# Kernel optimization log

Hardware: AMD Instinct MI355X
Metric: run time of the kernel (lower is better)

## Reference

```python
import jax, jax.numpy as jnp
import numpy as np

B, L1, L, DIM_IN, DIM_H, DIM_M = 8, 64, 1024, 512, 512, 512


def setup_inputs() -> dict:
    key = jax.random.key(0)
    ks = jax.random.split(key, 7)
    return {
        "query": jax.random.normal(ks[0], (L1, DIM_H), dtype=jnp.float32),
        "keys": jax.random.normal(ks[1], (B, L, DIM_IN), dtype=jnp.float32),
        "values": jax.random.normal(ks[2], (B, L, DIM_IN), dtype=jnp.float32),
        # nn.Linear weights: Wx (dim_middle, dim_in) no bias; Wh (dim_middle, dim_h) with bias; w (dim_middle,) no bias
        "Wx": jax.random.normal(ks[3], (DIM_M, DIM_IN), dtype=jnp.float32) * 0.02,
        "Wh": jax.random.normal(ks[4], (DIM_M, DIM_H), dtype=jnp.float32) * 0.02,
        "bh": jax.random.normal(ks[5], (DIM_M,), dtype=jnp.float32) * 0.02,
        "w": jax.random.normal(ks[6], (DIM_M,), dtype=jnp.float32) * 0.02,
    }


def reference(query, keys, values, Wx, Wh, bh, w):
    # mode='concept': query [l1, dh], keys/values [b, l, d]
    kx = jnp.einsum('bld,md->blm', keys, Wx)          # [b, l, m]
    qh = jnp.einsum('qd,md->qm', query, Wh) + bh       # [l1, m]
    g = jax.nn.relu(kx[:, None, :, :] + qh[None, :, None, :])  # [b, l1, l, m]
    scores = jnp.einsum('bqlm,m->bql', g, w)           # [b, l1, l]
    e = jax.nn.softmax(scores, axis=-1)                # softmax over key len (dim 2)
    return jnp.einsum('bql,bld->bqd', e, values)       # [b, l1, dv]
```

## Files before the change

kernel.cpp:

```cpp
#include <hip/hip_runtime.h>
#include <hip/hip_bf16.h>

#define BB 8
#define L1 64
#define LL 1024
#define DD 512

typedef float f32x4 __attribute__((ext_vector_type(4)));
typedef _Float16 f16;
typedef _Float16 f16x2 __attribute__((ext_vector_type(2)));
typedef _Float16 f16x4 __attribute__((ext_vector_type(4)));
typedef _Float16 f16x8 __attribute__((ext_vector_type(8)));

union F16x8u { f16x8 v; f16x2 h[4]; };

__global__ __launch_bounds__(256, 2) void kxqh_kernel(
    const float* __restrict__ keys,
    const float* __restrict__ query,
    const float* __restrict__ Wx,
    const float* __restrict__ Wh,
    const float* __restrict__ bh,
    f16* __restrict__ kx,
    f16* __restrict__ qh) {
  __shared__ char lds[24576] __attribute__((aligned(128)));
  const int t = threadIdx.x;
  const int lane = t & 63;
  const int w = t >> 6;
  const int wr = w >> 1, wc = w & 1;
  const int fq = lane >> 4, fr = lane & 15;
  const int bid = blockIdx.x;
  const bool isQH = (bid >= 512);
  const int rt = isQH ? 0 : (bid & 63);
  const int mt = isQH ? (bid - 512) : (bid >> 6);
  const int rowA0 = rt * 128;
  const int m0 = mt * 64;
  const float* Ap = isQH ? query : keys;
  const float* Wp = isQH ? Wh : Wx;

  f32x4 acc[4][2] = {};
  float4 ra[8], rb[4];

#define LOADK(K0)                                                              \
  do {                                                                         \
    _Pragma("unroll") for (int i = 0; i < 8; ++i) {                            \
      int flat = t * 4 + i * 1024;                                             \
      int row = flat >> 6, col = flat & 63;                                    \
      int arow = isQH ? (row & 63) : (rowA0 + row);                            \
      ra[i] = *reinterpret_cast<const float4*>(Ap + (size_t)arow * DD + (K0) + col); \
    }                                                                          \
    _Pragma("unroll") for (int i = 0; i < 4; ++i) {                            \
      int flat = t * 4 + i * 1024;                                             \
      int row = flat >> 6, col = flat & 63;                                    \
      rb[i] = *reinterpret_cast<const float4*>(Wp + (size_t)(m0 + row) * DD + (K0) + col); \
    }                                                                          \
  } while (0)

  LOADK(0);
  for (int s = 0; s < 8; ++s) {
    #pragma unroll
    for (int i = 0; i < 8; ++i) {
      int flat = t * 4 + i * 1024;
      int row = flat >> 6, col = flat & 63;
      f16x4 ha;
      ha[0] = (f16)ra[i].x; ha[1] = (f16)ra[i].y; ha[2] = (f16)ra[i].z; ha[3] = (f16)ra[i].w;
      int byte = (row * 128 + col * 2) ^ ((row & 7) << 4);
      *reinterpret_cast<f16x4*>(lds + byte) = ha;
    }
    #pragma unroll
    for (int i = 0; i < 4; ++i) {
      int flat = t * 4 + i * 1024;
      int row = flat >> 6, col = flat & 63;
      f16x4 hb;
      hb[0] = (f16)rb[i].x; hb[1] = (f16)rb[i].y; hb[2] = (f16)rb[i].z; hb[3] = (f16)rb[i].w;
      int byte = 16384 + ((row * 128 + col * 2) ^ ((row & 7) << 4));
      *reinterpret_cast<f16x4*>(lds + byte) = hb;
    }
    if (s < 7) LOADK((s + 1) * 64);
    __syncthreads();
    #pragma unroll
    for (int kh = 0; kh < 2; ++kh) {
      f16x8 af[4], bf[2];
      #pragma unroll
      for (int mi = 0; mi < 4; ++mi) {
        int row = wr * 64 + mi * 16 + fr;
        int byte = (row * 128 + kh * 64 + fq * 16) ^ ((row & 7) << 4);
        af[mi] = *reinterpret_cast<const f16x8*>(lds + byte);
      }
      #pragma unroll
      for (int ni = 0; ni < 2; ++ni) {
        int row = wc * 32 + ni * 16 + fr;
        int byte = 16384 + ((row * 128 + kh * 64 + fq * 16) ^ ((row & 7) << 4));
        bf[ni] = *reinterpret_cast<const f16x8*>(lds + byte);
      }
      #pragma unroll
      for (int mi = 0; mi < 4; ++mi)
        #pragma unroll
        for (int ni = 0; ni < 2; ++ni)
          acc[mi][ni] = __builtin_amdgcn_mfma_f32_16x16x32_f16(
              af[mi], bf[ni], acc[mi][ni], 0, 0, 0);
    }
    __syncthreads();
  }
#undef LOADK
  if (isQH) {
    #pragma unroll
    for (int mi = 0; mi < 4; ++mi) {
      #pragma unroll
      for (int ni = 0; ni < 2; ++ni) {
        int row = wr * 64 + mi * 16 + fq * 4;
        int col = m0 + wc * 32 + ni * 16 + fr;
        if (row < 64) {
          float bias = bh[col];
          #pragma unroll
          for (int r = 0; r < 4; ++r)
            qh[(size_t)(row + r) * DD + col] = (f16)(acc[mi][ni][r] + bias);
        }
      }
    }
  } else {
    #pragma unroll
    for (int mi = 0; mi < 4; ++mi) {
      #pragma unroll
      for (int ni = 0; ni < 2; ++ni) {
        int row = rowA0 + wr * 64 + mi * 16 + fq * 4;
        int col = m0 + wc * 32 + ni * 16 + fr;
        #pragma unroll
        for (int r = 0; r < 4; ++r)
          kx[(size_t)(row + r) * DD + col] = (f16)acc[mi][ni][r];
      }
    }
  }
}

__global__ __launch_bounds__(256, 2) void score4_kernel(
    const f16* __restrict__ kx,
    const f16* __restrict__ qh,
    const float* __restrict__ w,
    float* __restrict__ sc,
    float* __restrict__ pmax) {
  const int b = blockIdx.x & 7;
  const int l0 = (blockIdx.x >> 3) * 32;
  const int t = threadIdx.x;
  __shared__ __align__(16) f16 kxs[32][136];
  __shared__ __align__(16) f16 qhs[64][136];
  __shared__ __align__(16) f16 wsf[DD];
  __shared__ float smax[64][17];
  if (t < 128) {
    float4 wv = *reinterpret_cast<const float4*>(w + t * 4);
    f16x4 hv; hv[0] = (f16)wv.x; hv[1] = (f16)wv.y; hv[2] = (f16)wv.z; hv[3] = (f16)wv.w;
    *reinterpret_cast<f16x4*>(&wsf[t * 4]) = hv;
  }
  const int qb = t & 15;
  const int lt = (t >> 4) * 2;
  float acc[2][4] = {};
  uint4 rkx[2], rqh[4];

#define LOADM(M0)                                                              \
  do {                                                                         \
    _Pragma("unroll") for (int p = 0; p < 2; ++p) {                            \
      int flat = t * 8 + p * 2048;                                             \
      int row = flat >> 7, col = flat & 127;                                   \
      rkx[p] = *reinterpret_cast<const uint4*>(kx + (size_t)(b * LL + l0 + row) * DD + (M0) + col); \
    }                                                                          \
    _Pragma("unroll") for (int p = 0; p < 4; ++p) {                            \
      int flat = t * 8 + p * 2048;                                             \
      int row = flat >> 7, col = flat & 127;                                   \
      rqh[p] = *reinterpret_cast<const uint4*>(qh + (size_t)row * DD + (M0) + col); \
    }                                                                          \
  } while (0)

  LOADM(0);
  for (int m0 = 0; m0 < DD; m0 += 128) {
    #pragma unroll
    for (int p = 0; p < 2; ++p) {
      int flat = t * 8 + p * 2048;
      int row = flat >> 7, col = flat & 127;
      *reinterpret_cast<uint4*>(&kxs[row][col]) = rkx[p];
    }
    #pragma unroll
    for (int p = 0; p < 4; ++p) {
      int flat = t * 8 + p * 2048;
      int row = flat >> 7, col = flat & 127;
      *reinterpret_cast<uint4*>(&qhs[row][col]) = rqh[p];
    }
    if (m0 < DD - 128) LOADM(m0 + 128);
    __syncthreads();
    #pragma unroll 2
    for (int mm = 0; mm < 128; mm += 8) {
      F16x8u kv0, kv1, wv;
      kv0.v = *reinterpret_cast<const f16x8*>(&kxs[lt][mm]);
      kv1.v = *reinterpret_cast<const f16x8*>(&kxs[lt + 1][mm]);
      wv.v = *reinterpret_cast<const f16x8*>(&wsf[m0 + mm]);
      #pragma unroll
      for (int j = 0; j < 4; ++j) {
        F16x8u qv, g0, g1;
        qv.v = *reinterpret_cast<const f16x8*>(&qhs[qb + 16 * j][mm]);
        f16x8 zz = {};
        g0.v = __builtin_elementwise_max(kv0.v + qv.v, zz);
        g1.v = __builtin_elementwise_max(kv1.v + qv.v, zz);
        #pragma unroll
        for (int c = 0; c < 4; ++c) {
          acc[0][j] = __builtin_amdgcn_fdot2(g0.h[c], wv.h[c], acc[0][j], false);
          acc[1][j] = __builtin_amdgcn_fdot2(g1.h[c], wv.h[c], acc[1][j], false);
        }
      }
    }
    __syncthreads();
  }
#undef LOADM
  #pragma unroll
  for (int i = 0; i < 2; ++i)
    #pragma unroll
    for (int j = 0; j < 4; ++j)
      sc[((size_t)b * L1 + qb + 16 * j) * LL + l0 + lt + i] = acc[i][j];
  #pragma unroll
  for (int j = 0; j < 4; ++j)
    smax[qb + 16 * j][t >> 4] = fmaxf(acc[0][j], acc[1][j]);
  __syncthreads();
  if (t < 64) {
    float m = smax[t][0];
    #pragma unroll
    for (int i = 1; i < 16; ++i) m = fmaxf(m, smax[t][i]);
    pmax[((size_t)b * L1 + t) * 32 + (l0 >> 5)] = m;
  }
}

__global__ __launch_bounds__(256) void fso_kernel(
    const float* __restrict__ sc,
    const float* __restrict__ pmax,
    const float* __restrict__ v,
    float* __restrict__ out) {
  __shared__ __align__(16) char es[64 * 256];
  __shared__ __align__(16) char vt[16 * 256];
  __shared__ float rowm[64];
  __shared__ float rowinv[64];
  __shared__ float spart[64][17];
  const int t = threadIdx.x;
  const int lane = t & 63;
  const int w = t >> 6;
  const int fq = lane >> 4, fr = lane & 15;
  const int bid = blockIdx.x;
  const int b = bid & 7;
  const int d0 = (bid >> 3) * 16;
  const float* scb = sc + (size_t)b * L1 * LL;
  const float* vb = v + (size_t)b * LL * DD;

  const int eq = t >> 4;
  const int ec8 = t & 15;
  const int vl = t >> 1;
  const int vdh = (t & 1) * 8;
  float4 rsc[4][2];
  float4 rv[2];

#define LOADC(LC)                                                              \
  do {                                                                         \
    _Pragma("unroll") for (int p = 0; p < 4; ++p) {                            \
      const float* src = scb + (size_t)(eq + p * 16) * LL + (LC) * 128 + ec8 * 8; \
      rsc[p][0] = *reinterpret_cast<const float4*>(src);                       \
      rsc[p][1] = *reinterpret_cast<const float4*>(src + 4);                   \
    }                                                                          \
    const float* vsrc = vb + (size_t)((LC) * 128 + vl) * DD + d0 + vdh;        \
    rv[0] = *reinterpret_cast<const float4*>(vsrc);                            \
    rv[1] = *reinterpret_cast<const float4*>(vsrc + 4);                        \
  } while (0)

  LOADC(0);
  if (t < 64) {
    const float* pm = pmax + ((size_t)b * L1 + t) * 32;
    float4 m4 = *reinterpret_cast<const float4*>(pm);
    #pragma unroll
    for (int i = 1; i < 8; ++i) {
      float4 x = *reinterpret_cast<const float4*>(pm + i * 4);
      m4.x = fmaxf(m4.x, x.x); m4.y = fmaxf(m4.y, x.y);
      m4.z = fmaxf(m4.z, x.z); m4.w = fmaxf(m4.w, x.w);
    }
    rowm[t] = fmaxf(fmaxf(m4.x, m4.y), fmaxf(m4.z, m4.w));
  }
  __syncthreads();
  float rmv[4];
  #pragma unroll
  for (int p = 0; p < 4; ++p) rmv[p] = rowm[eq + p * 16];
  float spp[4] = {0.f, 0.f, 0.f, 0.f};
  f32x4 acc = {};

  for (int c = 0; c < 8; ++c) {
    #pragma unroll
    for (int p = 0; p < 4; ++p) {
      int q = eq + p * 16;
      float xs[8] = {rsc[p][0].x, rsc[p][0].y, rsc[p][0].z, rsc[p][0].w,
                     rsc[p][1].x, rsc[p][1].y, rsc[p][1].z, rsc[p][1].w};
      f16x8 h;
      #pragma unroll
      for (int j = 0; j < 8; ++j) {
        float e = __expf(xs[j] - rmv[p]);
        spp[p] += e;
        h[j] = (f16)e;
      }
      int byte = q * 256 + ((ec8 * 16) ^ ((q & 7) << 4));
      *reinterpret_cast<f16x8*>(es + byte) = h;
    }
    {
      float vs[8] = {rv[0].x, rv[0].y, rv[0].z, rv[0].w,
                     rv[1].x, rv[1].y, rv[1].z, rv[1].w};
      #pragma unroll
      for (int j = 0; j < 8; ++j) {
        int d = vdh + j;
        int byte = d * 256 + ((2 * vl) ^ ((d & 7) << 4));
        *reinterpret_cast<f16*>(vt + byte) = (f16)vs[j];
      }
    }
    if (c < 7) LOADC(c + 1);
    __syncthreads();
    #pragma unroll
    for (int ks = 0; ks < 4; ++ks) {
      int qa = w * 16 + fr;
      int colb = ks * 64 + fq * 16;
      f16x8 a = *reinterpret_cast<const f16x8*>(es + qa * 256 + (colb ^ ((qa & 7) << 4)));
      f16x8 bb = *reinterpret_cast<const f16x8*>(vt + fr * 256 + (colb ^ ((fr & 7) << 4)));
      acc = __builtin_amdgcn_mfma_f32_16x16x32_f16(a, bb, acc, 0, 0, 0);
    }
    __syncthreads();
  }
#undef LOADC
  #pragma unroll
  for (int p = 0; p < 4; ++p) spart[eq + p * 16][ec8] = spp[p];
  __syncthreads();
  if (t < 64) {
    float S = 0.f;
    #pragma unroll
    for (int i = 0; i < 16; ++i) S += spart[t][i];
    rowinv[t] = 1.f / S;
  }
  __syncthreads();
  #pragma unroll
  for (int r = 0; r < 4; ++r) {
    int q = w * 16 + fq * 4 + r;
    out[((size_t)b * L1 + q) * DD + d0 + fr] = acc[r] * rowinv[q];
  }
}

extern "C" void kernel_launch(void* const* d_in, const int* in_sizes, int n_in,
                              void* d_out, int out_size, void* d_ws, size_t ws_size,
                              hipStream_t stream) {
  const float* query  = (const float*)d_in[0];
  const float* keys   = (const float*)d_in[1];
  const float* values = (const float*)d_in[2];
  const float* Wx     = (const float*)d_in[3];
  const float* Wh     = (const float*)d_in[4];
  const float* bh     = (const float*)d_in[5];
  const float* w      = (const float*)d_in[6];
  float* out = (float*)d_out;

  char* ws = (char*)d_ws;
  f16*   kx   = (f16*)ws;
  f16*   qh   = (f16*)(ws + 8388608);
  float* sc   = (float*)(ws + 8454144);
  float* pmax = (float*)(ws + 10551296);

  kxqh_kernel<<<520, 256, 0, stream>>>(keys, query, Wx, Wh, bh, kx, qh);
  score4_kernel<<<BB * (LL / 32), 256, 0, stream>>>(kx, qh, w, sc, pmax);
  fso_kernel<<<256, 256, 0, stream>>>(sc, pmax, values, out);
}
```

Before: 59.50 us.

## Fuse keys projection into score kernel, split small qh GEMM into own kernel

```diff
diff --git a/kernel.cpp b/kernel.cpp
--- a/kernel.cpp
+++ b/kernel.cpp
@@ -14,187 +14,193 @@
 
 union F16x8u { f16x8 v; f16x2 h[4]; };
 
-__global__ __launch_bounds__(256, 2) void kxqh_kernel(
-    const float* __restrict__ keys,
+__global__ __launch_bounds__(256) void qh_kernel(
     const float* __restrict__ query,
-    const float* __restrict__ Wx,
     const float* __restrict__ Wh,
     const float* __restrict__ bh,
-    f16* __restrict__ kx,
     f16* __restrict__ qh) {
-  __shared__ char lds[24576] __attribute__((aligned(128)));
+  __shared__ char lds[18432] __attribute__((aligned(128)));
   const int t = threadIdx.x;
   const int lane = t & 63;
-  const int w = t >> 6;
-  const int wr = w >> 1, wc = w & 1;
+  const int wid = t >> 6;
   const int fq = lane >> 4, fr = lane & 15;
-  const int bid = blockIdx.x;
-  const bool isQH = (bid >= 512);
-  const int rt = isQH ? 0 : (bid & 63);
-  const int mt = isQH ? (bid - 512) : (bid >> 6);
-  const int rowA0 = rt * 128;
-  const int m0 = mt * 64;
-  const float* Ap = isQH ? query : keys;
-  const float* Wp = isQH ? Wh : Wx;
-
-  f32x4 acc[4][2] = {};
-  float4 ra[8], rb[4];
-
-#define LOADK(K0)                                                              \
+  const int m0 = blockIdx.x * 64;
+  f32x4 acc[4] = {};
+  float4 rq[4], rw[4];
+
+#define LOADQ(KC)                                                              \
   do {                                                                         \
-    _Pragma("unroll") for (int i = 0; i < 8; ++i) {                            \
-      int flat = t * 4 + i * 1024;                                             \
-      int row = flat >> 6, col = flat & 63;                                    \
-      int arow = isQH ? (row & 63) : (rowA0 + row);                            \
-      ra[i] = *reinterpret_cast<const float4*>(Ap + (size_t)arow * DD + (K0) + col); \
-    }                                                                          \
     _Pragma("unroll") for (int i = 0; i < 4; ++i) {                            \
-      int flat = t * 4 + i * 1024;                                             \
-      int row = flat >> 6, col = flat & 63;                                    \
-      rb[i] = *reinterpret_cast<const float4*>(Wp + (size_t)(m0 + row) * DD + (K0) + col); \
+      int slot = t + i * 256;                                                  \
+      int row = slot >> 4, c4 = (slot & 15) * 4;                               \
+      rq[i] = *reinterpret_cast<const float4*>(query + (size_t)row * DD + (KC)*64 + c4); \
+      rw[i] = *reinterpret_cast<const float4*>(Wh + (size_t)(m0 + row) * DD + (KC)*64 + c4); \
     }                                                                          \
   } while (0)
 
-  LOADK(0);
-  for (int s = 0; s < 8; ++s) {
-    #pragma unroll
-    for (int i = 0; i < 8; ++i) {
-      int flat = t * 4 + i * 1024;
-      int row = flat >> 6, col = flat & 63;
-      f16x4 ha;
-      ha[0] = (f16)ra[i].x; ha[1] = (f16)ra[i].y; ha[2] = (f16)ra[i].z; ha[3] = (f16)ra[i].w;
-      int byte = (row * 128 + col * 2) ^ ((row & 7) << 4);
-      *reinterpret_cast<f16x4*>(lds + byte) = ha;
-    }
+  LOADQ(0);
+  for (int kc = 0; kc < 8; ++kc) {
     #pragma unroll
     for (int i = 0; i < 4; ++i) {
-      int flat = t * 4 + i * 1024;
-      int row = flat >> 6, col = flat & 63;
-      f16x4 hb;
-      hb[0] = (f16)rb[i].x; hb[1] = (f16)rb[i].y; hb[2] = (f16)rb[i].z; hb[3] = (f16)rb[i].w;
-      int byte = 16384 + ((row * 128 + col * 2) ^ ((row & 7) << 4));
-      *reinterpret_cast<f16x4*>(lds + byte) = hb;
-    }
-    if (s < 7) LOADK((s + 1) * 64);
+      int slot = t + i * 256;
+      int row = slot >> 4, c4 = (slot & 15) * 4;
+      f16x4 hq, hw;
+      hq[0] = (f16)rq[i].x; hq[1] = (f16)rq[i].y; hq[2] = (f16)rq[i].z; hq[3] = (f16)rq[i].w;
+      hw[0] = (f16)rw[i].x; hw[1] = (f16)rw[i].y; hw[2] = (f16)rw[i].z; hw[3] = (f16)rw[i].w;
+      *reinterpret_cast<f16x4*>(lds + row * 144 + c4 * 2) = hq;
+      *reinterpret_cast<f16x4*>(lds + 9216 + row * 144 + c4 * 2) = hw;
+    }
+    if (kc < 7) LOADQ(kc + 1);
     __syncthreads();
     #pragma unroll
     for (int kh = 0; kh < 2; ++kh) {
-      f16x8 af[4], bf[2];
-      #pragma unroll
-      for (int mi = 0; mi < 4; ++mi) {
-        int row = wr * 64 + mi * 16 + fr;
-        int byte = (row * 128 + kh * 64 + fq * 16) ^ ((row & 7) << 4);
-        af[mi] = *reinterpret_cast<const f16x8*>(lds + byte);
-      }
-      #pragma unroll
-      for (int ni = 0; ni < 2; ++ni) {
-        int row = wc * 32 + ni * 16 + fr;
-        int byte = 16384 + ((row * 128 + kh * 64 + fq * 16) ^ ((row & 7) << 4));
-        bf[ni] = *reinterpret_cast<const f16x8*>(lds + byte);
-      }
-      #pragma unroll
-      for (int mi = 0; mi < 4; ++mi)
-        #pragma unroll
-        for (int ni = 0; ni < 2; ++ni)
-          acc[mi][ni] = __builtin_amdgcn_mfma_f32_16x16x32_f16(
-              af[mi], bf[ni], acc[mi][ni], 0, 0, 0);
-    }
-    __syncthreads();
-  }
-#undef LOADK
-  if (isQH) {
-    #pragma unroll
-    for (int mi = 0; mi < 4; ++mi) {
-      #pragma unroll
-      for (int ni = 0; ni < 2; ++ni) {
-        int row = wr * 64 + mi * 16 + fq * 4;
-        int col = m0 + wc * 32 + ni * 16 + fr;
-        if (row < 64) {
-          float bias = bh[col];
-          #pragma unroll
-          for (int r = 0; r < 4; ++r)
-            qh[(size_t)(row + r) * DD + col] = (f16)(acc[mi][ni][r] + bias);
-        }
-      }
-    }
-  } else {
-    #pragma unroll
-    for (int mi = 0; mi < 4; ++mi) {
-      #pragma unroll
-      for (int ni = 0; ni < 2; ++ni) {
-        int row = rowA0 + wr * 64 + mi * 16 + fq * 4;
-        int col = m0 + wc * 32 + ni * 16 + fr;
-        #pragma unroll
-        for (int r = 0; r < 4; ++r)
-          kx[(size_t)(row + r) * DD + col] = (f16)acc[mi][ni][r];
-      }
-    }
+      f16x8 bf = *reinterpret_cast<const f16x8*>(
+          lds + 9216 + (wid * 16 + fr) * 144 + kh * 64 + fq * 16);
+      #pragma unroll
+      for (int qf = 0; qf < 4; ++qf) {
+        f16x8 af = *reinterpret_cast<const f16x8*>(
+            lds + (qf * 16 + fr) * 144 + kh * 64 + fq * 16);
+        acc[qf] = __builtin_amdgcn_mfma_f32_16x16x32_f16(af, bf, acc[qf], 0, 0, 0);
+      }
+    }
+    __syncthreads();
+  }
+#undef LOADQ
+  #pragma unroll
+  for (int qf = 0; qf < 4; ++qf) {
+    int m = m0 + wid * 16 + fr;
+    float bias = bh[m];
+    #pragma unroll
+    for (int r = 0; r < 4; ++r)
+      qh[(size_t)(qf * 16 + fq * 4 + r) * DD + m] = (f16)(acc[qf][r] + bias);
   }
 }
 
-__global__ __launch_bounds__(256, 2) void score4_kernel(
-    const f16* __restrict__ kx,
+#define KEYSH_OFF 0
+#define WXS_OFF   32768
+#define QHS_OFF   32768
+#define KXS_OFF   51200
+#define WSF_OFF   59904
+#define SMAX_OFF  60928
+
+__global__ __launch_bounds__(256) void kscore_kernel(
+    const float* __restrict__ keys,
     const f16* __restrict__ qh,
+    const float* __restrict__ Wx,
     const float* __restrict__ w,
     float* __restrict__ sc,
     float* __restrict__ pmax) {
+  __shared__ char lds[63232] __attribute__((aligned(128)));
+  const int t = threadIdx.x;
+  const int lane = t & 63;
+  const int wid = t >> 6;
+  const int fq = lane >> 4, fr = lane & 15;
   const int b = blockIdx.x & 7;
   const int l0 = (blockIdx.x >> 3) * 32;
-  const int t = threadIdx.x;
-  __shared__ __align__(16) f16 kxs[32][136];
-  __shared__ __align__(16) f16 qhs[64][136];
-  __shared__ __align__(16) f16 wsf[DD];
-  __shared__ float smax[64][17];
+  const int qb = t & 15;
+  const int lq = t >> 4;
+
+  #pragma unroll
+  for (int j = 0; j < 16; ++j) {
+    int slot = t + j * 256;
+    int l = slot >> 7, kcol = (slot & 127) * 4;
+    float4 kv = *reinterpret_cast<const float4*>(
+        keys + (size_t)(b * LL + l0 + l) * DD + kcol);
+    f16x4 h;
+    h[0] = (f16)kv.x; h[1] = (f16)kv.y; h[2] = (f16)kv.z; h[3] = (f16)kv.w;
+    *reinterpret_cast<f16x4*>(
+        lds + KEYSH_OFF + l * 1024 + ((kcol * 2) ^ ((l & 7) << 4))) = h;
+  }
   if (t < 128) {
     float4 wv = *reinterpret_cast<const float4*>(w + t * 4);
     f16x4 hv; hv[0] = (f16)wv.x; hv[1] = (f16)wv.y; hv[2] = (f16)wv.z; hv[3] = (f16)wv.w;
-    *reinterpret_cast<f16x4*>(&wsf[t * 4]) = hv;
-  }
-  const int qb = t & 15;
-  const int lt = (t >> 4) * 2;
-  float acc[2][4] = {};
-  uint4 rkx[2], rqh[4];
-
-#define LOADM(M0)                                                              \
+    *reinterpret_cast<f16x4*>(lds + WSF_OFF + t * 8) = hv;
+  }
+
+  float4 rb[8];
+#define LOADW(MC, KC)                                                          \
   do {                                                                         \
-    _Pragma("unroll") for (int p = 0; p < 2; ++p) {                            \
-      int flat = t * 8 + p * 2048;                                             \
-      int row = flat >> 7, col = flat & 127;                                   \
-      rkx[p] = *reinterpret_cast<const uint4*>(kx + (size_t)(b * LL + l0 + row) * DD + (M0) + col); \
-    }                                                                          \
-    _Pragma("unroll") for (int p = 0; p < 4; ++p) {                            \
-      int flat = t * 8 + p * 2048;                                             \
-      int row = flat >> 7, col = flat & 127;                                   \
-      rqh[p] = *reinterpret_cast<const uint4*>(qh + (size_t)row * DD + (M0) + col); \
+    _Pragma("unroll") for (int i = 0; i < 8; ++i) {                            \
+      int slot = t + i * 256;                                                  \
+      int m = slot >> 4, c4 = (slot & 15) * 4;                                 \
+      rb[i] = *reinterpret_cast<const float4*>(                                \
+          Wx + (size_t)((MC) * 128 + m) * DD + (KC) * 64 + c4);                \
     }                                                                          \
   } while (0)
 
-  LOADM(0);
-  for (int m0 = 0; m0 < DD; m0 += 128) {
-    #pragma unroll
-    for (int p = 0; p < 2; ++p) {
-      int flat = t * 8 + p * 2048;
-      int row = flat >> 7, col = flat & 127;
-      *reinterpret_cast<uint4*>(&kxs[row][col]) = rkx[p];
-    }
-    #pragma unroll
-    for (int p = 0; p < 4; ++p) {
-      int flat = t * 8 + p * 2048;
-      int row = flat >> 7, col = flat & 127;
-      *reinterpret_cast<uint4*>(&qhs[row][col]) = rqh[p];
-    }
-    if (m0 < DD - 128) LOADM(m0 + 128);
+  LOADW(0, 0);
+  float acc[2][4] = {};
+
+  for (int mc = 0; mc < 4; ++mc) {
+    f32x4 cacc[2][2] = {};
+    for (int kc = 0; kc < 8; ++kc) {
+      #pragma unroll
+      for (int i = 0; i < 8; ++i) {
+        int slot = t + i * 256;
+        int m = slot >> 4, c4 = (slot & 15) * 4;
+        f16x4 h;
+        h[0] = (f16)rb[i].x; h[1] = (f16)rb[i].y; h[2] = (f16)rb[i].z; h[3] = (f16)rb[i].w;
+        *reinterpret_cast<f16x4*>(lds + WXS_OFF + m * 144 + c4 * 2) = h;
+      }
+      {
+        int nmc = mc, nkc = kc + 1;
+        if (nkc == 8) { nmc++; nkc = 0; }
+        if (nmc < 4) LOADW(nmc, nkc);
+      }
+      __syncthreads();
+      #pragma unroll
+      for (int kh = 0; kh < 2; ++kh) {
+        f16x8 af[2], bf[2];
+        #pragma unroll
+        for (int lf = 0; lf < 2; ++lf) {
+          int l = lf * 16 + fr;
+          af[lf] = *reinterpret_cast<const f16x8*>(
+              lds + KEYSH_OFF + l * 1024 +
+              ((kc * 128 + kh * 64 + fq * 16) ^ ((l & 7) << 4)));
+        }
+        #pragma unroll
+        for (int mf = 0; mf < 2; ++mf)
+          bf[mf] = *reinterpret_cast<const f16x8*>(
+              lds + WXS_OFF + (wid * 32 + mf * 16 + fr) * 144 + kh * 64 + fq * 16);
+        #pragma unroll
+        for (int lf = 0; lf < 2; ++lf)
+          #pragma unroll
+          for (int mf = 0; mf < 2; ++mf)
+            cacc[lf][mf] = __builtin_amdgcn_mfma_f32_16x16x32_f16(
+                af[lf], bf[mf], cacc[lf][mf], 0, 0, 0);
+      }
+      __syncthreads();
+    }
+    #pragma unroll
+    for (int lf = 0; lf < 2; ++lf)
+      #pragma unroll
+      for (int mf = 0; mf < 2; ++mf)
+        #pragma unroll
+        for (int r = 0; r < 4; ++r) {
+          int l = lf * 16 + fq * 4 + r;
+          int m = wid * 32 + mf * 16 + fr;
+          *reinterpret_cast<f16*>(lds + KXS_OFF + l * 272 + m * 2) =
+              (f16)cacc[lf][mf][r];
+        }
+    #pragma unroll
+    for (int j = 0; j < 4; ++j) {
+      int slot = t + j * 256;
+      int row = slot >> 4, c8 = (slot & 15) * 8;
+      uint4 qv = *reinterpret_cast<const uint4*>(qh + (size_t)row * DD + mc * 128 + c8);
+      *reinterpret_cast<uint4*>(lds + QHS_OFF + row * 272 + c8 * 2) = qv;
+    }
     __syncthreads();
     #pragma unroll 2
     for (int mm = 0; mm < 128; mm += 8) {
       F16x8u kv0, kv1, wv;
-      kv0.v = *reinterpret_cast<const f16x8*>(&kxs[lt][mm]);
-      kv1.v = *reinterpret_cast<const f16x8*>(&kxs[lt + 1][mm]);
-      wv.v = *reinterpret_cast<const f16x8*>(&wsf[m0 + mm]);
+      kv0.v = *reinterpret_cast<const f16x8*>(lds + KXS_OFF + lq * 272 + mm * 2);
+      kv1.v = *reinterpret_cast<const f16x8*>(lds + KXS_OFF + (lq + 16) * 272 + mm * 2);
+      wv.v = *reinterpret_cast<const f16x8*>(lds + WSF_OFF + (mc * 128 + mm) * 2);
       #pragma unroll
       for (int j = 0; j < 4; ++j) {
         F16x8u qv, g0, g1;
-        qv.v = *reinterpret_cast<const f16x8*>(&qhs[qb + 16 * j][mm]);
+        qv.v = *reinterpret_cast<const f16x8*>(
+            lds + QHS_OFF + (qb + 16 * j) * 272 + mm * 2);
         f16x8 zz = {};
         g0.v = __builtin_elementwise_max(kv0.v + qv.v, zz);
         g1.v = __builtin_elementwise_max(kv1.v + qv.v, zz);
@@ -207,20 +213,23 @@
     }
     __syncthreads();
   }
-#undef LOADM
+#undef LOADW
   #pragma unroll
   for (int i = 0; i < 2; ++i)
     #pragma unroll
     for (int j = 0; j < 4; ++j)
-      sc[((size_t)b * L1 + qb + 16 * j) * LL + l0 + lt + i] = acc[i][j];
+      sc[((size_t)b * L1 + qb + 16 * j) * LL + l0 + lq + 16 * i] = acc[i][j];
   #pragma unroll
   for (int j = 0; j < 4; ++j)
-    smax[qb + 16 * j][t >> 4] = fmaxf(acc[0][j], acc[1][j]);
+    *reinterpret_cast<f16*>(lds + SMAX_OFF + ((qb + 16 * j) * 18 + lq) * 2) =
+        (f16)fmaxf(acc[0][j], acc[1][j]);
   __syncthreads();
   if (t < 64) {
-    float m = smax[t][0];
-    #pragma unroll
-    for (int i = 1; i < 16; ++i) m = fmaxf(m, smax[t][i]);
+    float m = -3.4e38f;
+    #pragma unroll
+    for (int i = 0; i < 16; ++i)
+      m = fmaxf(m, (float)*reinterpret_cast<const f16*>(
+                       lds + SMAX_OFF + (t * 18 + i) * 2));
     pmax[((size_t)b * L1 + t) * 32 + (l0 >> 5)] = m;
   }
 }
@@ -352,12 +361,11 @@
   float* out = (float*)d_out;
 
   char* ws = (char*)d_ws;
-  f16*   kx   = (f16*)ws;
-  f16*   qh   = (f16*)(ws + 8388608);
-  float* sc   = (float*)(ws + 8454144);
-  float* pmax = (float*)(ws + 10551296);
-
-  kxqh_kernel<<<520, 256, 0, stream>>>(keys, query, Wx, Wh, bh, kx, qh);
-  score4_kernel<<<BB * (LL / 32), 256, 0, stream>>>(kx, qh, w, sc, pmax);
+  f16*   qh   = (f16*)ws;
+  float* sc   = (float*)(ws + 65536);
+  float* pmax = (float*)(ws + 65536 + 2097152);
+
+  qh_kernel<<<8, 256, 0, stream>>>(query, Wh, bh, qh);
+  kscore_kernel<<<256, 256, 0, stream>>>(keys, qh, Wx, w, sc, pmax);
   fso_kernel<<<256, 256, 0, stream>>>(sc, pmax, values, out);
 }
```

New measurement: 58.69 us. Within noise of the previous version (-1.4%).

## Split qh projection into own kernel and enlarge kx GEMM tile with double-buffered LDS

Applied to the files above, without the earlier changes.

```diff
diff --git a/kernel.cpp b/kernel.cpp
--- a/kernel.cpp
+++ b/kernel.cpp
@@ -14,120 +14,145 @@
 
 union F16x8u { f16x8 v; f16x2 h[4]; };
 
-__global__ __launch_bounds__(256, 2) void kxqh_kernel(
-    const float* __restrict__ keys,
+__global__ __launch_bounds__(256) void qh_kernel(
     const float* __restrict__ query,
-    const float* __restrict__ Wx,
     const float* __restrict__ Wh,
     const float* __restrict__ bh,
-    f16* __restrict__ kx,
     f16* __restrict__ qh) {
-  __shared__ char lds[24576] __attribute__((aligned(128)));
+  __shared__ char lds[18432] __attribute__((aligned(128)));
+  const int t = threadIdx.x;
+  const int lane = t & 63;
+  const int wid = t >> 6;
+  const int fq = lane >> 4, fr = lane & 15;
+  const int m0 = blockIdx.x * 64;
+  f32x4 acc[4] = {};
+  float4 rq[4], rw[4];
+
+#define LOADQ(KC)                                                              \
+  do {                                                                         \
+    _Pragma("unroll") for (int i = 0; i < 4; ++i) {                            \
+      int slot = t + i * 256;                                                  \
+      int row = slot >> 4, c4 = (slot & 15) * 4;                               \
+      rq[i] = *reinterpret_cast<const float4*>(query + (size_t)row * DD + (KC)*64 + c4); \
+      rw[i] = *reinterpret_cast<const float4*>(Wh + (size_t)(m0 + row) * DD + (KC)*64 + c4); \
+    }                                                                          \
+  } while (0)
+
+  LOADQ(0);
+  for (int kc = 0; kc < 8; ++kc) {
+    #pragma unroll
+    for (int i = 0; i < 4; ++i) {
+      int slot = t + i * 256;
+      int row = slot >> 4, c4 = (slot & 15) * 4;
+      f16x4 hq, hw;
+      hq[0] = (f16)rq[i].x; hq[1] = (f16)rq[i].y; hq[2] = (f16)rq[i].z; hq[3] = (f16)rq[i].w;
+      hw[0] = (f16)rw[i].x; hw[1] = (f16)rw[i].y; hw[2] = (f16)rw[i].z; hw[3] = (f16)rw[i].w;
+      *reinterpret_cast<f16x4*>(lds + row * 144 + c4 * 2) = hq;
+      *reinterpret_cast<f16x4*>(lds + 9216 + row * 144 + c4 * 2) = hw;
+    }
+    if (kc < 7) LOADQ(kc + 1);
+    __syncthreads();
+    #pragma unroll
+    for (int kh = 0; kh < 2; ++kh) {
+      f16x8 bf = *reinterpret_cast<const f16x8*>(
+          lds + 9216 + (wid * 16 + fr) * 144 + kh * 64 + fq * 16);
+      #pragma unroll
+      for (int qf = 0; qf < 4; ++qf) {
+        f16x8 af = *reinterpret_cast<const f16x8*>(
+            lds + (qf * 16 + fr) * 144 + kh * 64 + fq * 16);
+        acc[qf] = __builtin_amdgcn_mfma_f32_16x16x32_f16(af, bf, acc[qf], 0, 0, 0);
+      }
+    }
+    __syncthreads();
+  }
+#undef LOADQ
+  #pragma unroll
+  for (int qf = 0; qf < 4; ++qf) {
+    int m = m0 + wid * 16 + fr;
+    float bias = bh[m];
+    #pragma unroll
+    for (int r = 0; r < 4; ++r)
+      qh[(size_t)(qf * 16 + fq * 4 + r) * DD + m] = (f16)(acc[qf][r] + bias);
+  }
+}
+
+__global__ __launch_bounds__(256) void kx_kernel(
+    const float* __restrict__ keys,
+    const float* __restrict__ Wx,
+    f16* __restrict__ kx) {
+  __shared__ char lds[65536] __attribute__((aligned(128)));
   const int t = threadIdx.x;
   const int lane = t & 63;
   const int w = t >> 6;
   const int wr = w >> 1, wc = w & 1;
   const int fq = lane >> 4, fr = lane & 15;
-  const int bid = blockIdx.x;
-  const bool isQH = (bid >= 512);
-  const int rt = isQH ? 0 : (bid & 63);
-  const int mt = isQH ? (bid - 512) : (bid >> 6);
+  const int rt = blockIdx.x & 63;
+  const int mt = blockIdx.x >> 6;
   const int rowA0 = rt * 128;
-  const int m0 = mt * 64;
-  const float* Ap = isQH ? query : keys;
-  const float* Wp = isQH ? Wh : Wx;
-
-  f32x4 acc[4][2] = {};
-  float4 ra[8], rb[4];
+  const int m0 = mt * 128;
+
+  f32x4 acc[4][4] = {};
+  float4 ra[8], rb[8];
 
 #define LOADK(K0)                                                              \
   do {                                                                         \
     _Pragma("unroll") for (int i = 0; i < 8; ++i) {                            \
       int flat = t * 4 + i * 1024;                                             \
       int row = flat >> 6, col = flat & 63;                                    \
-      int arow = isQH ? (row & 63) : (rowA0 + row);                            \
-      ra[i] = *reinterpret_cast<const float4*>(Ap + (size_t)arow * DD + (K0) + col); \
-    }                                                                          \
-    _Pragma("unroll") for (int i = 0; i < 4; ++i) {                            \
-      int flat = t * 4 + i * 1024;                                             \
-      int row = flat >> 6, col = flat & 63;                                    \
-      rb[i] = *reinterpret_cast<const float4*>(Wp + (size_t)(m0 + row) * DD + (K0) + col); \
+      ra[i] = *reinterpret_cast<const float4*>(keys + (size_t)(rowA0 + row) * DD + (K0) + col); \
+      rb[i] = *reinterpret_cast<const float4*>(Wx + (size_t)(m0 + row) * DD + (K0) + col); \
     }                                                                          \
   } while (0)
 
   LOADK(0);
   for (int s = 0; s < 8; ++s) {
+    const int base = (s & 1) * 32768;
     #pragma unroll
     for (int i = 0; i < 8; ++i) {
       int flat = t * 4 + i * 1024;
       int row = flat >> 6, col = flat & 63;
-      f16x4 ha;
+      f16x4 ha, hb;
       ha[0] = (f16)ra[i].x; ha[1] = (f16)ra[i].y; ha[2] = (f16)ra[i].z; ha[3] = (f16)ra[i].w;
+      hb[0] = (f16)rb[i].x; hb[1] = (f16)rb[i].y; hb[2] = (f16)rb[i].z; hb[3] = (f16)rb[i].w;
       int byte = (row * 128 + col * 2) ^ ((row & 7) << 4);
-      *reinterpret_cast<f16x4*>(lds + byte) = ha;
-    }
-    #pragma unroll
-    for (int i = 0; i < 4; ++i) {
-      int flat = t * 4 + i * 1024;
-      int row = flat >> 6, col = flat & 63;
-      f16x4 hb;
-      hb[0] = (f16)rb[i].x; hb[1] = (f16)rb[i].y; hb[2] = (f16)rb[i].z; hb[3] = (f16)rb[i].w;
-      int byte = 16384 + ((row * 128 + col * 2) ^ ((row & 7) << 4));
-      *reinterpret_cast<f16x4*>(lds + byte) = hb;
+      *reinterpret_cast<f16x4*>(lds + base + byte) = ha;
+      *reinterpret_cast<f16x4*>(lds + base + 16384 + byte) = hb;
     }
     if (s < 7) LOADK((s + 1) * 64);
     __syncthreads();
     #pragma unroll
     for (int kh = 0; kh < 2; ++kh) {
-      f16x8 af[4], bf[2];
+      f16x8 af[4], bf[4];
       #pragma unroll
       for (int mi = 0; mi < 4; ++mi) {
         int row = wr * 64 + mi * 16 + fr;
         int byte = (row * 128 + kh * 64 + fq * 16) ^ ((row & 7) << 4);
-        af[mi] = *reinterpret_cast<const f16x8*>(lds + byte);
-      }
-      #pragma unroll
-      for (int ni = 0; ni < 2; ++ni) {
-        int row = wc * 32 + ni * 16 + fr;
-        int byte = 16384 + ((row * 128 + kh * 64 + fq * 16) ^ ((row & 7) << 4));
-        bf[ni] = *reinterpret_cast<const f16x8*>(lds + byte);
+        af[mi] = *reinterpret_cast<const f16x8*>(lds + base + byte);
+      }
+      #pragma unroll
+      for (int ni = 0; ni < 4; ++ni) {
+        int row = wc * 64 + ni * 16 + fr;
+        int byte = (row * 128 + kh * 64 + fq * 16) ^ ((row & 7) << 4);
+        bf[ni] = *reinterpret_cast<const f16x8*>(lds + base + 16384 + byte);
       }
       #pragma unroll
       for (int mi = 0; mi < 4; ++mi)
         #pragma unroll
-        for (int ni = 0; ni < 2; ++ni)
+        for (int ni = 0; ni < 4; ++ni)
           acc[mi][ni] = __builtin_amdgcn_mfma_f32_16x16x32_f16(
               af[mi], bf[ni], acc[mi][ni], 0, 0, 0);
     }
-    __syncthreads();
   }
 #undef LOADK
-  if (isQH) {
-    #pragma unroll
-    for (int mi = 0; mi < 4; ++mi) {
-      #pragma unroll
-      for (int ni = 0; ni < 2; ++ni) {
-        int row = wr * 64 + mi * 16 + fq * 4;
-        int col = m0 + wc * 32 + ni * 16 + fr;
-        if (row < 64) {
-          float bias = bh[col];
-          #pragma unroll
-          for (int r = 0; r < 4; ++r)
-            qh[(size_t)(row + r) * DD + col] = (f16)(acc[mi][ni][r] + bias);
-        }
-      }
-    }
-  } else {
-    #pragma unroll
-    for (int mi = 0; mi < 4; ++mi) {
-      #pragma unroll
-      for (int ni = 0; ni < 2; ++ni) {
-        int row = rowA0 + wr * 64 + mi * 16 + fq * 4;
-        int col = m0 + wc * 32 + ni * 16 + fr;
-        #pragma unroll
-        for (int r = 0; r < 4; ++r)
-          kx[(size_t)(row + r) * DD + col] = (f16)acc[mi][ni][r];
-      }
+  #pragma unroll
+  for (int mi = 0; mi < 4; ++mi) {
+    #pragma unroll
+    for (int ni = 0; ni < 4; ++ni) {
+      int row = rowA0 + wr * 64 + mi * 16 + fq * 4;
+      int col = m0 + wc * 64 + ni * 16 + fr;
+      #pragma unroll
+      for (int r = 0; r < 4; ++r)
+        kx[(size_t)(row + r) * DD + col] = (f16)acc[mi][ni][r];
     }
   }
 }
@@ -357,7 +382,8 @@
   float* sc   = (float*)(ws + 8454144);
   float* pmax = (float*)(ws + 10551296);
 
-  kxqh_kernel<<<520, 256, 0, stream>>>(keys, query, Wx, Wh, bh, kx, qh);
+  qh_kernel<<<8, 256, 0, stream>>>(query, Wh, bh, qh);
+  kx_kernel<<<256, 256, 0, stream>>>(keys, Wx, kx);
   score4_kernel<<<BB * (LL / 32), 256, 0, stream>>>(kx, qh, w, sc, pmax);
   fso_kernel<<<256, 256, 0, stream>>>(sc, pmax, values, out);
 }
```

Result: slower. 62.36 us (+4.8%).
